# Kernel tuning notes

Hardware: AMD Instinct MI355X
Metric: run time of the kernel (lower is better)

## Reference

```python
import jax, jax.numpy as jnp
import numpy as np

K = 16  # neighbors

def setup_inputs() -> dict:
    key = jax.random.key(0)
    k1, k2, k3 = jax.random.split(key, 3)
    B, C_in, C_out, N = 4, 64, 64, 8192
    x = jax.random.normal(k1, (B, C_in, N), dtype=jnp.float32)
    coords = jax.random.normal(k2, (B, 3, N), dtype=jnp.float32)
    W = jax.random.normal(k3, (C_out, C_in), dtype=jnp.float32) * 0.05
    return {"x": x, "coords": coords, "W": W}


def _knn_indices(coords, k):
    # coords: [B, 3, N]; squared pairwise distances d[b,i,j] = ||c_i - c_j||^2
    sq = jnp.sum(coords * coords, axis=1)                      # [B, N]
    inner = jnp.einsum('bdi,bdj->bij', coords, coords)         # [B, N, N]
    dist = sq[:, :, None] + sq[:, None, :] - 2.0 * inner       # [B, N, N]
    # k smallest distances -> top_k of negated distances
    _, idx = jax.lax.top_k(-dist, k)                           # [B, N, k]
    return idx


def _gather_neighbors(x, idx):
    # x: [B, C, N], idx: [B, N, k] -> [B, C, N, k]
    return jax.vmap(lambda xb, ib: xb[:, ib])(x, idx)


def reference(x, coords, W):
    idx = _knn_indices(coords, K)                              # [B, N, k]
    knn_x = _gather_neighbors(x, idx)                          # [B, C_in, N, k]
    # PointwiseConv2D (1x1 conv, no bias) == channel matmul
    mlp = jnp.einsum('oc,bcnk->bonk', W, knn_x)                # [B, C_out, N, k]
    y = jnp.max(mlp, axis=-1)                                  # [B, C_out, N]
    return (y, coords)
```

## Files before the change

kernel.cpp:

```cpp
#include <hip/hip_runtime.h>

#define BB 4
#define NN 8192
#define QB 32
#define NW 8
#define CAP 96
#define SLACK 6e-3f

typedef unsigned long long u64;
typedef unsigned int u32;
typedef _Float16 f16x8 __attribute__((ext_vector_type(8)));
typedef float f32x16 __attribute__((ext_vector_type(16)));

__device__ __forceinline__ u64 shfl_xor_u64(u64 v, int m) {
  u32 lo = (u32)v, hi = (u32)(v >> 32);
  lo = (u32)__shfl_xor((int)lo, m, 64);
  hi = (u32)__shfl_xor((int)hi, m, 64);
  return ((u64)hi << 32) | lo;
}
__device__ __forceinline__ u64 shfl_u64(u64 v, int src) {
  u32 lo = (u32)v, hi = (u32)(v >> 32);
  lo = (u32)__shfl((int)lo, src, 64);
  hi = (u32)__shfl((int)hi, src, 64);
  return ((u64)hi << 32) | lo;
}
__device__ __forceinline__ u64 min_u64(u64 a, u64 b) { return a < b ? a : b; }
__device__ __forceinline__ float rfl(float x) {
  return __int_as_float(__builtin_amdgcn_readfirstlane(__float_as_int(x)));
}

__device__ __forceinline__ u64 bitonic64(u64 v, int lane) {
#pragma unroll
  for (int k = 2; k <= 64; k <<= 1) {
#pragma unroll
    for (int jm = k >> 1; jm >= 1; jm >>= 1) {
      u64 o = shfl_xor_u64(v, jm);
      bool keepmin = ((lane & jm) == 0) == ((lane & k) == 0);
      u64 mn = min_u64(v, o);
      u64 mx = (v < o) ? o : v;
      v = keepmin ? mn : mx;
    }
  }
  return v;
}

__device__ __forceinline__ float dist_exact(float qx, float qy, float qz, float qw,
                                            float cx, float cy, float cz, float cw) {
#pragma clang fp contract(off)
  float inner = qx * cx;
  inner = inner + qy * cy;
  inner = inner + qz * cz;
  float tt = qw + cw;
  return __builtin_fmaf(-2.0f, inner, tt);
}

__global__ void __launch_bounds__(256, 4) fused_prep_zmat(
    const float* __restrict__ x, const float* __restrict__ W,
    const float* __restrict__ coords,
    float* __restrict__ z, float4* __restrict__ c4p,
    _Float16* __restrict__ bfr,
    float* __restrict__ ycoords) {
#pragma clang fp contract(off)
  __shared__ float Wst[64 * 68];
  __shared__ float xs[64 * 64];
  int t = threadIdx.x;
  if (blockIdx.x < 512) {
    int blk = blockIdx.x;
    int b = blk >> 7;
    int j0 = (blk & 127) * 64;
    for (int r = t; r < 4096; r += 256) Wst[(r & 63) * 68 + (r >> 6)] = W[r];
    const float* xb = x + (size_t)b * 64 * NN;
#pragma unroll
    for (int r = 0; r < 16; ++r) {
      int idx = t + r * 256;
      int c = idx >> 6, j = idx & 63;
      xs[c * 64 + j] = xb[(size_t)c * NN + j0 + j];
    }
    __syncthreads();
    int o0 = (t & 15) * 4, jb = (t >> 4) * 4;
    float4 a0 = {0.f, 0.f, 0.f, 0.f}, a1 = a0, a2 = a0, a3 = a0;
#pragma unroll 4
    for (int c = 0; c < 64; ++c) {
      float4 w4 = *(const float4*)&Wst[c * 68 + o0];
      float4 x4 = *(const float4*)&xs[c * 64 + jb];
      a0.x = __builtin_fmaf(w4.x, x4.x, a0.x);
      a0.y = __builtin_fmaf(w4.y, x4.x, a0.y);
      a0.z = __builtin_fmaf(w4.z, x4.x, a0.z);
      a0.w = __builtin_fmaf(w4.w, x4.x, a0.w);
      a1.x = __builtin_fmaf(w4.x, x4.y, a1.x);
      a1.y = __builtin_fmaf(w4.y, x4.y, a1.y);
      a1.z = __builtin_fmaf(w4.z, x4.y, a1.z);
      a1.w = __builtin_fmaf(w4.w, x4.y, a1.w);
      a2.x = __builtin_fmaf(w4.x, x4.z, a2.x);
      a2.y = __builtin_fmaf(w4.y, x4.z, a2.y);
      a2.z = __builtin_fmaf(w4.z, x4.z, a2.z);
      a2.w = __builtin_fmaf(w4.w, x4.z, a2.w);
      a3.x = __builtin_fmaf(w4.x, x4.w, a3.x);
      a3.y = __builtin_fmaf(w4.y, x4.w, a3.y);
      a3.z = __builtin_fmaf(w4.z, x4.w, a3.z);
      a3.w = __builtin_fmaf(w4.w, x4.w, a3.w);
    }
    size_t rbase = (size_t)b * NN + j0 + jb;
    *(float4*)&z[(rbase + 0) * 64 + o0] = a0;
    *(float4*)&z[(rbase + 1) * 64 + o0] = a1;
    *(float4*)&z[(rbase + 2) * 64 + o0] = a2;
    *(float4*)&z[(rbase + 3) * 64 + o0] = a3;
  } else {
    int t2 = (blockIdx.x - 512) * 256 + t;
    int b = t2 >> 13;
    int i = t2 & (NN - 1);
    const float* cb = coords + (size_t)b * 3 * NN;
    float cx = cb[i];
    float cy = cb[NN + i];
    float cz = cb[2 * NN + i];
    float sq = (cx * cx + cy * cy) + cz * cz;
    float4 v; v.x = -2.0f * cx; v.y = -2.0f * cy; v.z = -2.0f * cz; v.w = sq;
    c4p[t2] = v;

    _Float16 xh = (_Float16)v.x, yh = (_Float16)v.y, zh = (_Float16)v.z;
    _Float16 xl = (_Float16)(v.x - (float)xh);
    _Float16 yl = (_Float16)(v.y - (float)yh);
    _Float16 zl = (_Float16)(v.z - (float)zh);
    _Float16 sh = (_Float16)sq;
    _Float16 sl = (_Float16)(sq - (float)sh);
    f16x8 b0, b1;
    b0[0] = xh; b0[1] = xh; b0[2] = xl; b0[3] = yh;
    b0[4] = yh; b0[5] = yl; b0[6] = zh; b0[7] = zh;
    b1[0] = zl; b1[1] = sh; b1[2] = sl;
    b1[3] = (_Float16)0.f; b1[4] = (_Float16)0.f; b1[5] = (_Float16)0.f;
    b1[6] = (_Float16)0.f; b1[7] = (_Float16)0.f;
    f16x8* bp = (f16x8*)bfr;
    bp[(size_t)t2 * 2]     = b0;
    bp[(size_t)t2 * 2 + 1] = b1;

#pragma unroll
    for (int r = 0; r < 3; ++r)
      ycoords[r * (BB * NN) + t2] = coords[r * (BB * NN) + t2];
  }
}

__global__ void __launch_bounds__(512, 8) knn_gather(const float4* __restrict__ c4p,
                                                     const _Float16* __restrict__ bfr,
                                                     const float* __restrict__ z,
                                                     float* __restrict__ y) {
  __shared__ __align__(16) char pool[QB * 128 * 4];
  __shared__ float TfL[QB];
  __shared__ int scnt[QB];
  __shared__ int sidx[QB][16];
  __shared__ float ys[64][QB + 1];
  float (*wmin)[128] = (float(*)[128])pool;
  u32 (*survj)[CAP] = (u32(*)[CAP])pool;

  int t = threadIdx.x;
  int w = t >> 6, lane = t & 63;
  int lq = lane & 31, lg = lane >> 5;
  int lg4 = lg << 2;
  int qbase = blockIdx.x * QB;
  int b = qbase >> 13;
  int i0 = qbase & (NN - 1);
  const float4* cp = c4p + (size_t)b * NN;
  int wbase = w * (NN / NW);

  if (t < QB) scnt[t] = 0;

  float4 qv = cp[i0 + lq];
  float qx = -0.5f * qv.x, qy = -0.5f * qv.y, qz = -0.5f * qv.z;
  _Float16 xh = (_Float16)qx, yh = (_Float16)qy, zh = (_Float16)qz;
  _Float16 xl = (_Float16)(qx - (float)xh);
  _Float16 yl = (_Float16)(qy - (float)yh);
  _Float16 zl = (_Float16)(qz - (float)zh);
  f16x8 af;
  if (lg == 0) {
    af[0] = xh; af[1] = xl; af[2] = xh; af[3] = yh;
    af[4] = yl; af[5] = yh; af[6] = zh; af[7] = zl;
  } else {
    af[0] = zh; af[1] = (_Float16)1.0f; af[2] = (_Float16)1.0f;
    af[3] = (_Float16)0.f; af[4] = (_Float16)0.f; af[5] = (_Float16)0.f;
    af[6] = (_Float16)0.f; af[7] = (_Float16)0.f;
  }

  f32x16 zzz, mn;
#pragma unroll
  for (int r = 0; r < 16; ++r) { zzz[r] = 0.f; mn[r] = 3.402823466e+38f; }

  const f16x8* lp = (const f16x8*)bfr + (((size_t)b * NN + wbase + lq) * 2 + lg);

#pragma unroll 2
  for (int tt = 0; tt < 16; tt += 2) {
    f16x8 bc0 = lp[tt * 64];
    f16x8 bc1 = lp[(tt + 1) * 64];
    f32x16 d0 = __builtin_amdgcn_mfma_f32_32x32x16_f16(af, bc0, zzz, 0, 0, 0);
    f32x16 d1 = __builtin_amdgcn_mfma_f32_32x32x16_f16(af, bc1, zzz, 0, 0, 0);
#pragma unroll
    for (int r = 0; r < 16; ++r) mn[r] = fminf(fminf(mn[r], d0[r]), d1[r]);
  }

#pragma unroll
  for (int r = 0; r < 16; ++r) {
    float m2 = fminf(mn[r], __shfl_xor(mn[r], 16, 64));
    int q = (r & 3) + 8 * (r >> 2) + lg4;
    if (lq < 16) wmin[q][w * 16 + lq] = m2;
  }
  __syncthreads();

#pragma unroll 1
  for (int qi = 0; qi < QB / NW; ++qi) {
    int q = w * (QB / NW) + qi;
    float v = fminf(wmin[q][2 * lane], wmin[q][2 * lane + 1]);
#pragma unroll
    for (int k = 2; k <= 64; k <<= 1) {
#pragma unroll
      for (int jm = k >> 1; jm >= 1; jm >>= 1) {
        float o = __shfl_xor(v, jm, 64);
        bool keepmin = ((lane & jm) == 0) == ((lane & k) == 0);
        v = keepmin ? fminf(v, o) : fmaxf(v, o);
      }
    }
    if (lane == 15) TfL[q] = v + SLACK;
  }
  __syncthreads();

  f32x16 mc;
#pragma unroll
  for (int r = 0; r < 16; ++r) mc[r] = -TfL[(r & 3) + 8 * (r >> 2) + lg4];

#pragma unroll 4
  for (int tt = 0; tt < 32; ++tt) {
    f16x8 bc = lp[tt * 64];
    f32x16 d = __builtin_amdgcn_mfma_f32_32x32x16_f16(af, bc, mc, 0, 0, 0);
    int cand = wbase + tt * 32 + lq;
#pragma unroll
    for (int r = 0; r < 16; ++r) {
      if (d[r] <= 0.f) {
        int q = (r & 3) + 8 * (r >> 2) + lg4;
        int pos = atomicAdd(&scnt[q], 1);
        if (pos < CAP) survj[q][pos] = (u32)cand;
      }
    }
  }
  __syncthreads();

  const float* zb = z + (size_t)b * NN * 64;
#pragma unroll 1
  for (int qi = 0; qi < QB / NW; ++qi) {
    int q = w * (QB / NW) + qi;
    int n = scnt[q]; if (n > CAP) n = CAP;
    float4 qq = cp[i0 + q];
    float eqx = rfl(-0.5f * qq.x), eqy = rfl(-0.5f * qq.y);
    float eqz = rfl(-0.5f * qq.z), eqw = rfl(qq.w);
    u64 v = ~0ull;
    if (lane < n) {
      int c = (int)survj[q][lane];
      float4 cj = cp[c];
      float de = dist_exact(eqx, eqy, eqz, eqw,
                            -0.5f * cj.x, -0.5f * cj.y, -0.5f * cj.z, cj.w);
      u32 f = __float_as_uint(de);
      u32 m32 = f ^ ((u32)(((int)f) >> 31) | 0x80000000u);
      v = ((u64)m32 << 32) | (u32)c;
    }
    v = bitonic64(v, lane);
    if (n > 64) {
      u64 v2 = ~0ull;
      if (lane + 64 < n) {
        int c = (int)survj[q][lane + 64];
        float4 cj = cp[c];
        float de = dist_exact(eqx, eqy, eqz, eqw,
                              -0.5f * cj.x, -0.5f * cj.y, -0.5f * cj.z, cj.w);
        u32 f = __float_as_uint(de);
        u32 m32 = f ^ ((u32)(((int)f) >> 31) | 0x80000000u);
        v2 = ((u64)m32 << 32) | (u32)c;
      }
      v2 = bitonic64(v2, lane);
      u64 s2 = shfl_u64(v2, (lane + 48) & 63);
      u64 vm = (lane < 16) ? v : ((lane < 32) ? s2 : ~0ull);
      v = bitonic64(vm, lane);
    }
    if (lane < 16) sidx[q][lane] = (int)(v & 0xFFFFFFFFull);
  }

#pragma unroll 1
  for (int qi = 0; qi < QB / NW; ++qi) {
    int q = w * (QB / NW) + qi;
    const int* id = sidx[q];
    float m = -3.402823466e+38f;
#pragma unroll
    for (int k = 0; k < 16; ++k)
      m = fmaxf(m, zb[(size_t)id[k] * 64 + lane]);
    ys[lane][q] = m;
  }
  __syncthreads();
  {
    int o = t >> 3;
    int ql0 = (t & 7) * 4;
    float4 vv;
    vv.x = ys[o][ql0]; vv.y = ys[o][ql0 + 1];
    vv.z = ys[o][ql0 + 2]; vv.w = ys[o][ql0 + 3];
    *(float4*)&y[((size_t)b * 64 + o) * NN + i0 + ql0] = vv;
  }
}

extern "C" void kernel_launch(void* const* d_in, const int* in_sizes, int n_in,
                              void* d_out, int out_size, void* d_ws, size_t ws_size,
                              hipStream_t stream) {
  const float* x      = (const float*)d_in[0];
  const float* coords = (const float*)d_in[1];
  const float* W      = (const float*)d_in[2];
  float* y = (float*)d_out;

  char* ws = (char*)d_ws;
  float4*   c4p = (float4*)ws;
  _Float16* bfr = (_Float16*)(ws + (512u << 10));
  float*    z   = (float*)(ws + (2u << 20));

  float* ycoords = y + (size_t)BB * 64 * NN;

  fused_prep_zmat<<<512 + 128, 256, 0, stream>>>(x, W, coords, z, c4p, bfr, ycoords);
  knn_gather<<<BB * NN / QB, 512, 0, stream>>>(c4p, bfr, z, y);
}
```

Before: 136.9 us.

## Add 32-bit ballot top-16 fast path and widen threshold sampling pass

Top-16 selection now has a fast path. A 32-bit bitonic sort of the distance keys finds the 16th-smallest key, and ballots plus mbcnt scatter the winning indices straight into sidx. The older 64-bit key/index bitonic sort only runs for overflow cases or ties at the threshold. The MFMA threshold-estimation loop covers twice as many candidate tiles, which should give a tighter cutoff and fewer survivors but costs more MFMA work and loads. The neighbor gather-max now loads all 16 values before a tree reduction to expose memory parallelism, and two loops get more unrolling.

```diff
diff --git a/kernel.cpp b/kernel.cpp
--- a/kernel.cpp
+++ b/kernel.cpp
@@ -39,6 +39,19 @@
       u64 mn = min_u64(v, o);
       u64 mx = (v < o) ? o : v;
       v = keepmin ? mn : mx;
+    }
+  }
+  return v;
+}
+
+__device__ __forceinline__ u32 bitonic32v(u32 v, int lane) {
+#pragma unroll
+  for (int k = 2; k <= 64; k <<= 1) {
+#pragma unroll
+    for (int jm = k >> 1; jm >= 1; jm >>= 1) {
+      u32 o = (u32)__shfl_xor((int)v, jm, 64);
+      bool keepmin = ((lane & jm) == 0) == ((lane & k) == 0);
+      v = keepmin ? (v < o ? v : o) : (v < o ? o : v);
     }
   }
   return v;
@@ -186,7 +199,7 @@
   const f16x8* lp = (const f16x8*)bfr + (((size_t)b * NN + wbase + lq) * 2 + lg);
 
 #pragma unroll 2
-  for (int tt = 0; tt < 16; tt += 2) {
+  for (int tt = 0; tt < 32; tt += 2) {
     f16x8 bc0 = lp[tt * 64];
     f16x8 bc1 = lp[(tt + 1) * 64];
     f32x16 d0 = __builtin_amdgcn_mfma_f32_32x32x16_f16(af, bc0, zzz, 0, 0, 0);
@@ -203,7 +216,7 @@
   }
   __syncthreads();
 
-#pragma unroll 1
+#pragma unroll
   for (int qi = 0; qi < QB / NW; ++qi) {
     int q = w * (QB / NW) + qi;
     float v = fminf(wmin[q][2 * lane], wmin[q][2 * lane + 1]);
@@ -248,45 +261,63 @@
     float4 qq = cp[i0 + q];
     float eqx = rfl(-0.5f * qq.x), eqy = rfl(-0.5f * qq.y);
     float eqz = rfl(-0.5f * qq.z), eqw = rfl(qq.w);
-    u64 v = ~0ull;
+    u32 m32 = 0xFFFFFFFFu, idxv = 0u;
     if (lane < n) {
       int c = (int)survj[q][lane];
       float4 cj = cp[c];
       float de = dist_exact(eqx, eqy, eqz, eqw,
                             -0.5f * cj.x, -0.5f * cj.y, -0.5f * cj.z, cj.w);
       u32 f = __float_as_uint(de);
-      u32 m32 = f ^ ((u32)(((int)f) >> 31) | 0x80000000u);
-      v = ((u64)m32 << 32) | (u32)c;
-    }
-    v = bitonic64(v, lane);
-    if (n > 64) {
-      u64 v2 = ~0ull;
-      if (lane + 64 < n) {
-        int c = (int)survj[q][lane + 64];
-        float4 cj = cp[c];
-        float de = dist_exact(eqx, eqy, eqz, eqw,
-                              -0.5f * cj.x, -0.5f * cj.y, -0.5f * cj.z, cj.w);
-        u32 f = __float_as_uint(de);
-        u32 m32 = f ^ ((u32)(((int)f) >> 31) | 0x80000000u);
-        v2 = ((u64)m32 << 32) | (u32)c;
+      m32 = f ^ ((u32)(((int)f) >> 31) | 0x80000000u);
+      idxv = (u32)c;
+    }
+    u32 T15 = (u32)__shfl((int)bitonic32v(m32, lane), 15, 64);
+    u64 blt = __ballot(m32 < T15);
+    u64 beq = __ballot(m32 == T15);
+    int k2 = 16 - __popcll(blt);
+    if (n <= 64 && __popcll(beq) == k2) {
+      u64 sel = blt | beq;
+      if ((sel >> lane) & 1ull) {
+        int slot = __builtin_amdgcn_mbcnt_hi(
+            (u32)(sel >> 32), __builtin_amdgcn_mbcnt_lo((u32)sel, 0u));
+        sidx[q][slot] = (int)idxv;
       }
-      v2 = bitonic64(v2, lane);
-      u64 s2 = shfl_u64(v2, (lane + 48) & 63);
-      u64 vm = (lane < 16) ? v : ((lane < 32) ? s2 : ~0ull);
-      v = bitonic64(vm, lane);
-    }
-    if (lane < 16) sidx[q][lane] = (int)(v & 0xFFFFFFFFull);
-  }
-
-#pragma unroll 1
+    } else {
+      u64 v = (lane < n) ? (((u64)m32 << 32) | idxv) : ~0ull;
+      v = bitonic64(v, lane);
+      if (n > 64) {
+        u64 v2 = ~0ull;
+        if (lane + 64 < n) {
+          int c = (int)survj[q][lane + 64];
+          float4 cj = cp[c];
+          float de = dist_exact(eqx, eqy, eqz, eqw,
+                                -0.5f * cj.x, -0.5f * cj.y, -0.5f * cj.z, cj.w);
+          u32 f = __float_as_uint(de);
+          u32 mm = f ^ ((u32)(((int)f) >> 31) | 0x80000000u);
+          v2 = ((u64)mm << 32) | (u32)c;
+        }
+        v2 = bitonic64(v2, lane);
+        u64 s2 = shfl_u64(v2, (lane + 48) & 63);
+        u64 vm = (lane < 16) ? v : ((lane < 32) ? s2 : ~0ull);
+        v = bitonic64(vm, lane);
+      }
+      if (lane < 16) sidx[q][lane] = (int)(v & 0xFFFFFFFFull);
+    }
+  }
+
+#pragma unroll 2
   for (int qi = 0; qi < QB / NW; ++qi) {
     int q = w * (QB / NW) + qi;
     const int* id = sidx[q];
-    float m = -3.402823466e+38f;
+    float vv[16];
 #pragma unroll
     for (int k = 0; k < 16; ++k)
-      m = fmaxf(m, zb[(size_t)id[k] * 64 + lane]);
-    ys[lane][q] = m;
+      vv[k] = zb[(size_t)id[k] * 64 + lane];
+#pragma unroll
+    for (int s = 8; s >= 1; s >>= 1)
+#pragma unroll
+      for (int k = 0; k < s; ++k) vv[k] = fmaxf(vv[k], vv[k + s]);
+    ys[lane][q] = vv[0];
   }
   __syncthreads();
   {
```

Result: faster. 130.3 us (median of 2 runs) (-4.8%).
